# Kernel optimization log

Measured on AMD Instinct MI355X. Metric: run time of the kernel, lower is better.

## Reference

```python
import jax, jax.numpy as jnp
import numpy as np


def _soft_proto(x, P):
    d2 = (x * x).sum(-1, keepdims=True) - 2.0 * (x @ P.T) + (P * P).sum(-1)
    w = jax.nn.softmax(-d2, axis=-1)  # scores = -dist_sq, softmax over K
    return w @ P  # soft-matched prototypes


def setup_inputs() -> dict:
    key = jax.random.key(0)
    ks = jax.random.split(key, 12)
    B = 1024
    def u(k, shape, s=0.1):
        return jax.random.uniform(k, shape, minval=-s, maxval=s, dtype=jnp.float32)
    return {
        "fcn": jax.random.normal(ks[0], (B, 90, 90), jnp.float32),
        "scn": jax.random.normal(ks[1], (B, 90, 90), jnp.float32),
        # node embedding Linear(90->48), weights stored [in,out]
        "W_node": u(ks[2], (90, 48)), "b_node": jnp.zeros((48,), jnp.float32),
        "P_node": u(ks[3], (64, 48)),   # node prototypes, init uniform(-0.1,0.1)
        "W_graph": u(ks[4], (48, 32)), "b_graph": jnp.zeros((32,), jnp.float32),
        "P_graph": u(ks[5], (32, 32)),
        "Wg1": u(ks[6], (32, 32)), "bg1": jnp.zeros((32,), jnp.float32),
        "Wg2": u(ks[7], (32, 16)), "bg2": jnp.zeros((16,), jnp.float32),
        "P_cls": u(ks[8], (16, 16)),
        # classifier: final_dim = 2*90*48 + 2*32 + 2*16 = 8736
        "Wc1": u(ks[9], (8736, 256)), "bc1": jnp.zeros((256,), jnp.float32),
        "Wc2": u(ks[10], (256, 3)), "bc2": jnp.zeros((3,), jnp.float32),
    }


def reference(fcn, scn, W_node, b_node, P_node, W_graph, b_graph, P_graph,
              Wg1, bg1, Wg2, bg2, P_cls, Wc1, bc1, Wc2, bc2):
    def branch(x):
        nodes = x @ W_node + b_node                  # [B,90,48]
        nm = _soft_proto(nodes, P_node)              # [B,90,48]
        eg = nm.mean(axis=1) @ W_graph + b_graph     # [B,32]
        gp = _soft_proto(eg, P_graph)                # [B,32]
        ec = jax.nn.relu(gp @ Wg1 + bg1) @ Wg2 + bg2 # [B,16]
        cp = _soft_proto(ec, P_cls)                  # [B,16]
        return nm, gp, cp

    nmf, gpf, cpf = branch(fcn)
    nms, gps, cps = branch(scn)
    B = fcn.shape[0]
    R = jnp.concatenate(
        [nmf.reshape(B, -1), nms.reshape(B, -1), gpf, gps, cpf, cps], axis=-1)  # [B,8736]
    # dropout(0.5) is identity in eval mode
    logits = jax.nn.relu(R @ Wc1 + bc1) @ Wc2 + bc2  # [B,3]
    return logits
```

## Files before the change

### kernel.cpp

```cpp
#include <hip/hip_runtime.h>
#include <hip/hip_bf16.h>

using f16   = _Float16;
using f16x4 = __attribute__((ext_vector_type(4))) _Float16;
using f16x8 = __attribute__((ext_vector_type(8))) _Float16;
using f32x4 = __attribute__((ext_vector_type(4))) float;

__global__ __launch_bounds__(256) void prep_kernel(
    const float* __restrict__ Wn, const float* __restrict__ Pn,
    f16* __restrict__ wf, float* __restrict__ q)
{
  int i = blockIdx.x * 256 + threadIdx.x;
  if (i < 4992) {
    int n = i / 104, k = i - n * 104;
    wf[i] = (k < 90) ? (f16)Wn[k * 48 + n] : (f16)0.f;
  } else if (i < 8576) {
    int j = i - 4992; int p = j / 56, c = j - p * 56;
    wf[i] = (c < 48) ? (f16)Pn[p * 48 + c] : (f16)0.f;
  } else if (i < 12032) {
    int j = i - 8576; int r = j / 72, p = j - r * 72;
    wf[i] = (p < 64) ? (f16)Pn[p * 48 + r] : (f16)0.f;
  } else if (i < 12096) {
    int p = i - 12032;
    float s = 0.f;
    for (int j = 0; j < 48; ++j) { float v = Pn[p * 48 + j]; s = fmaf(v, v, s); }
    q[p] = s;
  }
}

__global__ __launch_bounds__(256) void wc1t_kernel(
    const float* __restrict__ Wc1, f16* __restrict__ Wc1T)
{
  __shared__ f16 sT[32 * 36];
  const int tid = threadIdx.x;
  const int kt = blockIdx.x, ct = blockIdx.y;
  const int c = tid & 31, r4 = (tid >> 5) * 4;
  #pragma unroll
  for (int i = 0; i < 4; ++i) {
    int r = r4 + i;
    sT[c * 36 + r] = (f16)Wc1[(size_t)(kt * 32 + r) * 256 + ct * 32 + c];
  }
  __syncthreads();
  #pragma unroll
  for (int i = 0; i < 4; ++i) {
    int r = r4 + i;
    Wc1T[(size_t)(ct * 32 + r) * 8736 + kt * 32 + c] = sT[r * 36 + c];
  }
}

__global__ __launch_bounds__(384) void node_kernel(
    const float* __restrict__ fcn, const float* __restrict__ scn,
    const float* __restrict__ bn, const f16* __restrict__ wf,
    const float* __restrict__ qg,
    f16* __restrict__ R, float* __restrict__ nmmean)
{
  __shared__ __align__(16) f16 sWt[12032];
  __shared__ __align__(16) f16 sS[6][1152];
  __shared__ float sCol[6][3][16];

  f16* sWnT = sWt;
  f16* sP   = sWt + 4992;
  f16* sPnT = sWt + 8576;

  const int tid = threadIdx.x;
  const int lane = tid & 63, wv = tid >> 6;
  const int l15 = lane & 15, lg = lane >> 4;
  const int b = blockIdx.x, br = blockIdx.y;
  const float* x = (br ? scn : fcn) + (size_t)b * 8100;
  f16* scr = sS[wv];

  const int row = wv * 16 + l15;
  const float* xrow = x + row * 90;
  float2 xl[3][4];
  #pragma unroll
  for (int kt = 0; kt < 3; ++kt) {
    #pragma unroll
    for (int e = 0; e < 4; ++e) xl[kt][e] = make_float2(0.f, 0.f);
    const int k0 = kt * 32 + lg * 8;
    if (row < 90) {
      const float* src = xrow + k0;
      if (k0 < 88) {
        xl[kt][0] = *(const float2*)(src + 0);
        xl[kt][1] = *(const float2*)(src + 2);
        xl[kt][2] = *(const float2*)(src + 4);
        xl[kt][3] = *(const float2*)(src + 6);
      } else {
        xl[kt][0] = *(const float2*)src;
      }
    }
  }

  for (int i = tid; i < 1504; i += 384)
    ((f16x8*)sWt)[i] = ((const f16x8*)wf)[i];
  __syncthreads();

  f16x8 a[3];
  #pragma unroll
  for (int kt = 0; kt < 3; ++kt) {
    f16x8 h;
    h[0] = (f16)xl[kt][0].x; h[1] = (f16)xl[kt][0].y;
    h[2] = (f16)xl[kt][1].x; h[3] = (f16)xl[kt][1].y;
    h[4] = (f16)xl[kt][2].x; h[5] = (f16)xl[kt][2].y;
    h[6] = (f16)xl[kt][3].x; h[7] = (f16)xl[kt][3].y;
    a[kt] = h;
  }

  #pragma unroll
  for (int nt = 0; nt < 3; ++nt) {
    f32x4 acc = {0.f, 0.f, 0.f, 0.f};
    #pragma unroll
    for (int kt = 0; kt < 3; ++kt) {
      f16x8 bb = *(const f16x8*)&sWnT[(nt * 16 + l15) * 104 + kt * 32 + lg * 8];
      acc = __builtin_amdgcn_mfma_f32_16x16x32_f16(a[kt], bb, acc, 0, 0, 0);
    }
    const float bias = bn[nt * 16 + l15];
    #pragma unroll
    for (int r = 0; r < 4; ++r)
      scr[(lg * 4 + r) * 56 + nt * 16 + l15] = (f16)(acc[r] + bias);
  }
  asm volatile("s_waitcnt lgkmcnt(0)" ::: "memory");
  __builtin_amdgcn_sched_barrier(0);

  const f16x8 a0 = *(const f16x8*)&scr[l15 * 56 + lg * 8];
  const f16x4 a1 = *(const f16x4*)&scr[l15 * 56 + 32 + lg * 4];
  f32x4 acc2[4];
  #pragma unroll
  for (int nt = 0; nt < 4; ++nt) acc2[nt] = (f32x4){0.f, 0.f, 0.f, 0.f};
  #pragma unroll
  for (int nt = 0; nt < 4; ++nt) {
    f16x8 b0 = *(const f16x8*)&sP[(nt * 16 + l15) * 56 + lg * 8];
    acc2[nt] = __builtin_amdgcn_mfma_f32_16x16x32_f16(a0, b0, acc2[nt], 0, 0, 0);
    f16x4 b1 = *(const f16x4*)&sP[(nt * 16 + l15) * 56 + 32 + lg * 4];
    acc2[nt] = __builtin_amdgcn_mfma_f32_16x16x16f16(a1, b1, acc2[nt], 0, 0, 0);
  }
  float qv[4];
  #pragma unroll
  for (int nt = 0; nt < 4; ++nt) qv[nt] = qg[nt * 16 + l15];
  #pragma unroll
  for (int r = 0; r < 4; ++r) {
    float s0 = 2.f * acc2[0][r] - qv[0];
    float s1 = 2.f * acc2[1][r] - qv[1];
    float s2 = 2.f * acc2[2][r] - qv[2];
    float s3 = 2.f * acc2[3][r] - qv[3];
    float m = fmaxf(fmaxf(s0, s1), fmaxf(s2, s3));
    m = fmaxf(m, __shfl_xor(m, 1, 64));
    m = fmaxf(m, __shfl_xor(m, 2, 64));
    m = fmaxf(m, __shfl_xor(m, 4, 64));
    m = fmaxf(m, __shfl_xor(m, 8, 64));
    float e0 = __expf(s0 - m), e1 = __expf(s1 - m);
    float e2 = __expf(s2 - m), e3 = __expf(s3 - m);
    float sum = (e0 + e1) + (e2 + e3);
    sum += __shfl_xor(sum, 1, 64);
    sum += __shfl_xor(sum, 2, 64);
    sum += __shfl_xor(sum, 4, 64);
    sum += __shfl_xor(sum, 8, 64);
    const float inv = 1.f / sum;
    const int lr = lg * 4 + r;
    scr[lr * 72 + 0 * 16 + l15] = (f16)(e0 * inv);
    scr[lr * 72 + 1 * 16 + l15] = (f16)(e1 * inv);
    scr[lr * 72 + 2 * 16 + l15] = (f16)(e2 * inv);
    scr[lr * 72 + 3 * 16 + l15] = (f16)(e3 * inv);
  }
  asm volatile("s_waitcnt lgkmcnt(0)" ::: "memory");
  __builtin_amdgcn_sched_barrier(0);

  f16* Rrow = R + (size_t)b * 8736 + (size_t)br * 4320;
  const f16x8 wa0 = *(const f16x8*)&scr[l15 * 72 + lg * 8];
  const f16x8 wa1 = *(const f16x8*)&scr[l15 * 72 + 32 + lg * 8];
  float cs[3] = {0.f, 0.f, 0.f};
  #pragma unroll
  for (int nt = 0; nt < 3; ++nt) {
    f32x4 acc = {0.f, 0.f, 0.f, 0.f};
    f16x8 b0 = *(const f16x8*)&sPnT[(nt * 16 + l15) * 72 + lg * 8];
    acc = __builtin_amdgcn_mfma_f32_16x16x32_f16(wa0, b0, acc, 0, 0, 0);
    f16x8 b1 = *(const f16x8*)&sPnT[(nt * 16 + l15) * 72 + 32 + lg * 8];
    acc = __builtin_amdgcn_mfma_f32_16x16x32_f16(wa1, b1, acc, 0, 0, 0);
    #pragma unroll
    for (int r = 0; r < 4; ++r) {
      const int grow = wv * 16 + lg * 4 + r;
      if (grow < 90) {
        Rrow[grow * 48 + nt * 16 + l15] = (f16)acc[r];
        cs[nt] += acc[r];
      }
    }
  }
  #pragma unroll
  for (int nt = 0; nt < 3; ++nt) {
    cs[nt] += __shfl_xor(cs[nt], 16, 64);
    cs[nt] += __shfl_xor(cs[nt], 32, 64);
  }
  if (lane < 16) {
    sCol[wv][0][lane] = cs[0];
    sCol[wv][1][lane] = cs[1];
    sCol[wv][2][lane] = cs[2];
  }
  __syncthreads();
  if (tid < 48) {
    const int nt = tid >> 4, c = tid & 15;
    float s = 0.f;
    #pragma unroll
    for (int w = 0; w < 6; ++w) s += sCol[w][nt][c];
    nmmean[((size_t)br * 1024 + b) * 48 + tid] = s * (1.f / 90.f);
  }
}

__global__ __launch_bounds__(256) void graph_kernel(
    const float* __restrict__ nmmean,
    const float* __restrict__ Wg, const float* __restrict__ bg,
    const float* __restrict__ Pg,
    const float* __restrict__ Wg1, const float* __restrict__ bg1,
    const float* __restrict__ Wg2, const float* __restrict__ bg2,
    const float* __restrict__ Pc,
    f16* __restrict__ R)
{
  __shared__ float sE[4][64];
  __shared__ float sT[4][64];
  const int tid = threadIdx.x;
  const int wid = tid >> 6, lane = tid & 63;
  const int idx = blockIdx.x * 4 + wid;
  const int br = idx >> 10, b = idx & 1023;
  const float* mrow = nmmean + (size_t)idx * 48;
  f16* Rrow = R + (size_t)b * 8736;

  if (lane < 32) {
    float e = bg[lane];
    #pragma unroll
    for (int k = 0; k < 48; ++k) e = fmaf(mrow[k], Wg[k * 32 + lane], e);
    sE[wid][lane] = e;
  }
  __syncthreads();
  if (lane < 32) {
    float s = 0.f;
    #pragma unroll
    for (int j = 0; j < 32; ++j) { float pv = Pg[lane * 32 + j]; s += pv * (2.f * sE[wid][j] - pv); }
    float m = s;
    for (int d = 16; d >= 1; d >>= 1) m = fmaxf(m, __shfl_xor(m, d, 64));
    float ex = __expf(s - m);
    float sum = ex;
    for (int d = 16; d >= 1; d >>= 1) sum += __shfl_xor(sum, d, 64);
    sT[wid][lane] = ex / sum;
  }
  __syncthreads();
  if (lane < 32) {
    float g = 0.f;
    #pragma unroll
    for (int p = 0; p < 32; ++p) g = fmaf(sT[wid][p], Pg[p * 32 + lane], g);
    Rrow[8640 + br * 32 + lane] = (f16)g;
    sE[wid][lane] = g;
  }
  __syncthreads();
  if (lane < 32) {
    float h = bg1[lane];
    #pragma unroll
    for (int k = 0; k < 32; ++k) h = fmaf(sE[wid][k], Wg1[k * 32 + lane], h);
    sT[wid][lane] = fmaxf(h, 0.f);
  }
  __syncthreads();
  if (lane < 16) {
    float c = bg2[lane];
    #pragma unroll
    for (int k = 0; k < 32; ++k) c = fmaf(sT[wid][k], Wg2[k * 16 + lane], c);
    sE[wid][lane] = c;
  }
  __syncthreads();
  if (lane < 16) {
    float s = 0.f;
    #pragma unroll
    for (int j = 0; j < 16; ++j) { float pv = Pc[lane * 16 + j]; s += pv * (2.f * sE[wid][j] - pv); }
    float m = s;
    for (int d = 8; d >= 1; d >>= 1) m = fmaxf(m, __shfl_xor(m, d, 64));
    float ex = __expf(s - m);
    float sum = ex;
    for (int d = 8; d >= 1; d >>= 1) sum += __shfl_xor(sum, d, 64);
    sT[wid][lane] = ex / sum;
  }
  __syncthreads();
  if (lane < 16) {
    float c = 0.f;
    #pragma unroll
    for (int p = 0; p < 16; ++p) c = fmaf(sT[wid][p], Pc[p * 16 + lane], c);
    Rrow[8704 + br * 16 + lane] = (f16)c;
  }
}

__global__ __launch_bounds__(256) void gemm1_kernel(
    const f16* __restrict__ R, const f16* __restrict__ Wc1T,
    float* __restrict__ part, int KS)
{
  __shared__ __align__(16) f16 sA[128 * 40];
  __shared__ __align__(16) f16 sB[64 * 40];
  const int tid = threadIdx.x;
  const int lane = tid & 63, wv = tid >> 6;
  const int l15 = lane & 15, lg = lane >> 4;
  const int wm = wv >> 1, wn = wv & 1;
  const int bm = blockIdx.x * 128, bnc = blockIdx.y * 64, z = blockIdx.z;
  const int base = 273 / KS, rem = 273 - base * KS;
  const int t0 = z * base + (z < rem ? z : rem);
  const int nt_ = base + (z < rem ? 1 : 0);
  const int kbeg = t0 * 32, kend = (t0 + nt_) * 32;

  const int ar = tid >> 1, ah = (tid & 1) * 16;
  const int bc = tid >> 2, bh = (tid & 3) * 8;

  f32x4 acc[4][2];
  #pragma unroll
  for (int mt = 0; mt < 4; ++mt)
    #pragma unroll
    for (int nt = 0; nt < 2; ++nt) acc[mt][nt] = (f32x4){0.f, 0.f, 0.f, 0.f};

  f16x8 v0 = *(const f16x8*)&R[(size_t)(bm + ar) * 8736 + kbeg + ah];
  f16x8 v1 = *(const f16x8*)&R[(size_t)(bm + ar) * 8736 + kbeg + ah + 8];
  f16x8 w0 = *(const f16x8*)&Wc1T[(size_t)(bnc + bc) * 8736 + kbeg + bh];

  for (int kk = kbeg; kk < kend; kk += 32) {
    *(f16x8*)&sA[ar * 40 + ah] = v0;
    *(f16x8*)&sA[ar * 40 + ah + 8] = v1;
    *(f16x8*)&sB[bc * 40 + bh] = w0;
    __syncthreads();
    if (kk + 32 < kend) {
      v0 = *(const f16x8*)&R[(size_t)(bm + ar) * 8736 + kk + 32 + ah];
      v1 = *(const f16x8*)&R[(size_t)(bm + ar) * 8736 + kk + 32 + ah + 8];
      w0 = *(const f16x8*)&Wc1T[(size_t)(bnc + bc) * 8736 + kk + 32 + bh];
    }
    #pragma unroll
    for (int mt = 0; mt < 4; ++mt) {
      f16x8 a = *(const f16x8*)&sA[(wm * 64 + mt * 16 + l15) * 40 + lg * 8];
      #pragma unroll
      for (int nt = 0; nt < 2; ++nt) {
        f16x8 bb = *(const f16x8*)&sB[(wn * 32 + nt * 16 + l15) * 40 + lg * 8];
        acc[mt][nt] = __builtin_amdgcn_mfma_f32_16x16x32_f16(a, bb, acc[mt][nt], 0, 0, 0);
      }
    }
    __syncthreads();
  }
  float* pz = part + (size_t)z * 262144;
  #pragma unroll
  for (int mt = 0; mt < 4; ++mt)
    #pragma unroll
    for (int nt = 0; nt < 2; ++nt)
      #pragma unroll
      for (int r = 0; r < 4; ++r)
        pz[(size_t)(bm + wm * 64 + mt * 16 + lg * 4 + r) * 256 +
           bnc + wn * 32 + nt * 16 + l15] = acc[mt][nt][r];
}

__global__ __launch_bounds__(256) void head_kernel(
    const float* __restrict__ part, const float* __restrict__ bc1,
    const float* __restrict__ Wc2, const float* __restrict__ bc2,
    float* __restrict__ out, int KS)
{
  __shared__ float red[3][4];
  const int b = blockIdx.x, t = threadIdx.x;
  float s0 = 0.f, s1 = 0.f, s2 = 0.f, s3 = 0.f;
  int z = 0;
  for (; z + 4 <= KS; z += 4) {
    s0 += part[(size_t)(z + 0) * 262144 + (size_t)b * 256 + t];
    s1 += part[(size_t)(z + 1) * 262144 + (size_t)b * 256 + t];
    s2 += part[(size_t)(z + 2) * 262144 + (size_t)b * 256 + t];
    s3 += part[(size_t)(z + 3) * 262144 + (size_t)b * 256 + t];
  }
  for (; z < KS; ++z) s0 += part[(size_t)z * 262144 + (size_t)b * 256 + t];
  float acc = bc1[t] + ((s0 + s1) + (s2 + s3));
  float h = fmaxf(acc, 0.f);
  float p0 = h * Wc2[t * 3 + 0];
  float p1 = h * Wc2[t * 3 + 1];
  float p2 = h * Wc2[t * 3 + 2];
  for (int d = 32; d >= 1; d >>= 1) {
    p0 += __shfl_xor(p0, d, 64);
    p1 += __shfl_xor(p1, d, 64);
    p2 += __shfl_xor(p2, d, 64);
  }
  const int wid = t >> 6, lane = t & 63;
  if (lane == 0) { red[0][wid] = p0; red[1][wid] = p1; red[2][wid] = p2; }
  __syncthreads();
  if (t < 3) {
    out[(size_t)b * 3 + t] = red[t][0] + red[t][1] + red[t][2] + red[t][3] + bc2[t];
  }
}

extern "C" void kernel_launch(void* const* d_in, const int* in_sizes, int n_in,
                              void* d_out, int out_size, void* d_ws, size_t ws_size,
                              hipStream_t stream) {
  const float* fcn     = (const float*)d_in[0];
  const float* scn     = (const float*)d_in[1];
  const float* W_node  = (const float*)d_in[2];
  const float* b_node  = (const float*)d_in[3];
  const float* P_node  = (const float*)d_in[4];
  const float* W_graph = (const float*)d_in[5];
  const float* b_graph = (const float*)d_in[6];
  const float* P_graph = (const float*)d_in[7];
  const float* Wg1     = (const float*)d_in[8];
  const float* bg1     = (const float*)d_in[9];
  const float* Wg2     = (const float*)d_in[10];
  const float* bg2     = (const float*)d_in[11];
  const float* P_cls   = (const float*)d_in[12];
  const float* Wc1     = (const float*)d_in[13];
  const float* bc1     = (const float*)d_in[14];
  const float* Wc2     = (const float*)d_in[15];
  const float* bc2     = (const float*)d_in[16];
  float* out = (float*)d_out;

  char* ws = (char*)d_ws;
  f16*   R16    = (f16*)ws;
  f16*   Wc1T   = (f16*)(ws + 17891328);
  f16*   wf     = (f16*)(ws + 22364160);
  float* qbuf   = (float*)(ws + 22388224);
  float* nmmean = (float*)(ws + 22388480);
  float* part   = (float*)(ws + 22781696);

  size_t avail = ws_size > 22781696u ? ws_size - 22781696u : 0;
  int KS = (int)(avail / 1048576u);
  if (KS > 16) KS = 16;
  if (KS < 1) KS = 1;

  prep_kernel<<<48, 256, 0, stream>>>(W_node, P_node, wf, qbuf);
  wc1t_kernel<<<dim3(273, 8), 256, 0, stream>>>(Wc1, Wc1T);
  node_kernel<<<dim3(1024, 2), 384, 0, stream>>>(fcn, scn, b_node, wf, qbuf,
                                                 R16, nmmean);
  graph_kernel<<<512, 256, 0, stream>>>(nmmean, W_graph, b_graph, P_graph,
                                        Wg1, bg1, Wg2, bg2, P_cls, R16);
  gemm1_kernel<<<dim3(8, 4, KS), 256, 0, stream>>>(R16, Wc1T, part, KS);
  head_kernel<<<1024, 256, 0, stream>>>(part, bc1, Wc2, bc2, out, KS);
}
```

Baseline: 68.61 us.

## Merge independent kernels into horizontal fat launches and move graph/cls terms to head

Merges the Wc1 transpose into the node kernel as extra blocks, and the graph/proto kernel into the split-K GEMM kernel as extra blocks. This removes launches and lets independent work share the GPU. To break the dependency of the GEMM on the graph outputs, the GEMM now covers only the first 270 K-tiles (the node features). The remaining 96 classifier columns are computed in fp32 inside the head kernel from a new gcp buffer. The transpose blocks now run with 384-thread blocks where only 256 threads work, and the head kernel does extra strided Wc1 reads per row.

Measured after the change: 68.61 us. No clear change (-0.0%).

```diff
diff --git a/kernel.cpp b/kernel.cpp
--- a/kernel.cpp
+++ b/kernel.cpp
@@ -28,44 +28,49 @@
   }
 }
 
-__global__ __launch_bounds__(256) void wc1t_kernel(
-    const float* __restrict__ Wc1, f16* __restrict__ Wc1T)
-{
-  __shared__ f16 sT[32 * 36];
-  const int tid = threadIdx.x;
-  const int kt = blockIdx.x, ct = blockIdx.y;
-  const int c = tid & 31, r4 = (tid >> 5) * 4;
-  #pragma unroll
-  for (int i = 0; i < 4; ++i) {
-    int r = r4 + i;
-    sT[c * 36 + r] = (f16)Wc1[(size_t)(kt * 32 + r) * 256 + ct * 32 + c];
-  }
-  __syncthreads();
-  #pragma unroll
-  for (int i = 0; i < 4; ++i) {
-    int r = r4 + i;
-    Wc1T[(size_t)(ct * 32 + r) * 8736 + kt * 32 + c] = sT[r * 36 + c];
-  }
-}
-
-__global__ __launch_bounds__(384) void node_kernel(
+__global__ __launch_bounds__(384) void fat1_kernel(
     const float* __restrict__ fcn, const float* __restrict__ scn,
     const float* __restrict__ bn, const f16* __restrict__ wf,
     const float* __restrict__ qg,
+    const float* __restrict__ Wc1, f16* __restrict__ Wc1T,
     f16* __restrict__ R, float* __restrict__ nmmean)
 {
   __shared__ __align__(16) f16 sWt[12032];
   __shared__ __align__(16) f16 sS[6][1152];
   __shared__ float sCol[6][3][16];
 
+  const int blk = blockIdx.x;
+  const int tid = threadIdx.x;
+
+  if (blk < 2184) {
+    f16* sT = sWt;
+    const int kt = blk % 273, ct = blk / 273;
+    const int c = tid & 31, r4 = (tid >> 5) * 4;
+    if (tid < 256) {
+      #pragma unroll
+      for (int i = 0; i < 4; ++i) {
+        int r = r4 + i;
+        sT[c * 36 + r] = (f16)Wc1[(size_t)(kt * 32 + r) * 256 + ct * 32 + c];
+      }
+    }
+    __syncthreads();
+    if (tid < 256) {
+      #pragma unroll
+      for (int i = 0; i < 4; ++i) {
+        int r = r4 + i;
+        Wc1T[(size_t)(ct * 32 + r) * 8736 + kt * 32 + c] = sT[r * 36 + c];
+      }
+    }
+    return;
+  }
+
+  const int unit = blk - 2184;
+  const int b = unit & 1023, br = unit >> 10;
   f16* sWnT = sWt;
   f16* sP   = sWt + 4992;
   f16* sPnT = sWt + 8576;
-
-  const int tid = threadIdx.x;
   const int lane = tid & 63, wv = tid >> 6;
   const int l15 = lane & 15, lg = lane >> 4;
-  const int b = blockIdx.x, br = blockIdx.y;
   const float* x = (br ? scn : fcn) + (size_t)b * 8100;
   f16* scr = sS[wv];
 
@@ -204,97 +209,102 @@
   }
 }
 
-__global__ __launch_bounds__(256) void graph_kernel(
+__global__ __launch_bounds__(256) void fat2_kernel(
     const float* __restrict__ nmmean,
     const float* __restrict__ Wg, const float* __restrict__ bg,
     const float* __restrict__ Pg,
     const float* __restrict__ Wg1, const float* __restrict__ bg1,
     const float* __restrict__ Wg2, const float* __restrict__ bg2,
     const float* __restrict__ Pc,
-    f16* __restrict__ R)
-{
-  __shared__ float sE[4][64];
-  __shared__ float sT[4][64];
-  const int tid = threadIdx.x;
-  const int wid = tid >> 6, lane = tid & 63;
-  const int idx = blockIdx.x * 4 + wid;
-  const int br = idx >> 10, b = idx & 1023;
-  const float* mrow = nmmean + (size_t)idx * 48;
-  f16* Rrow = R + (size_t)b * 8736;
-
-  if (lane < 32) {
-    float e = bg[lane];
-    #pragma unroll
-    for (int k = 0; k < 48; ++k) e = fmaf(mrow[k], Wg[k * 32 + lane], e);
-    sE[wid][lane] = e;
-  }
-  __syncthreads();
-  if (lane < 32) {
-    float s = 0.f;
-    #pragma unroll
-    for (int j = 0; j < 32; ++j) { float pv = Pg[lane * 32 + j]; s += pv * (2.f * sE[wid][j] - pv); }
-    float m = s;
-    for (int d = 16; d >= 1; d >>= 1) m = fmaxf(m, __shfl_xor(m, d, 64));
-    float ex = __expf(s - m);
-    float sum = ex;
-    for (int d = 16; d >= 1; d >>= 1) sum += __shfl_xor(sum, d, 64);
-    sT[wid][lane] = ex / sum;
-  }
-  __syncthreads();
-  if (lane < 32) {
-    float g = 0.f;
-    #pragma unroll
-    for (int p = 0; p < 32; ++p) g = fmaf(sT[wid][p], Pg[p * 32 + lane], g);
-    Rrow[8640 + br * 32 + lane] = (f16)g;
-    sE[wid][lane] = g;
-  }
-  __syncthreads();
-  if (lane < 32) {
-    float h = bg1[lane];
-    #pragma unroll
-    for (int k = 0; k < 32; ++k) h = fmaf(sE[wid][k], Wg1[k * 32 + lane], h);
-    sT[wid][lane] = fmaxf(h, 0.f);
-  }
-  __syncthreads();
-  if (lane < 16) {
-    float c = bg2[lane];
-    #pragma unroll
-    for (int k = 0; k < 32; ++k) c = fmaf(sT[wid][k], Wg2[k * 16 + lane], c);
-    sE[wid][lane] = c;
-  }
-  __syncthreads();
-  if (lane < 16) {
-    float s = 0.f;
-    #pragma unroll
-    for (int j = 0; j < 16; ++j) { float pv = Pc[lane * 16 + j]; s += pv * (2.f * sE[wid][j] - pv); }
-    float m = s;
-    for (int d = 8; d >= 1; d >>= 1) m = fmaxf(m, __shfl_xor(m, d, 64));
-    float ex = __expf(s - m);
-    float sum = ex;
-    for (int d = 8; d >= 1; d >>= 1) sum += __shfl_xor(sum, d, 64);
-    sT[wid][lane] = ex / sum;
-  }
-  __syncthreads();
-  if (lane < 16) {
-    float c = 0.f;
-    #pragma unroll
-    for (int p = 0; p < 16; ++p) c = fmaf(sT[wid][p], Pc[p * 16 + lane], c);
-    Rrow[8704 + br * 16 + lane] = (f16)c;
-  }
-}
-
-__global__ __launch_bounds__(256) void gemm1_kernel(
+    float* __restrict__ gcp,
     const f16* __restrict__ R, const f16* __restrict__ Wc1T,
     float* __restrict__ part, int KS)
 {
   __shared__ __align__(16) f16 sA[128 * 40];
   __shared__ __align__(16) f16 sB[64 * 40];
+
+  const int blk = blockIdx.x;
   const int tid = threadIdx.x;
+
+  if (blk < 512) {
+    float (*sE)[64] = (float(*)[64])sA;
+    float (*sT)[64] = (float(*)[64])(sA + 512);
+    const int wid = tid >> 6, lane = tid & 63;
+    const int idx = blk * 4 + wid;
+    const int br = idx >> 10, b = idx & 1023;
+    const float* mrow = nmmean + (size_t)idx * 48;
+    float* grow = gcp + (size_t)idx * 48;
+
+    if (lane < 32) {
+      float e = bg[lane];
+      #pragma unroll
+      for (int k = 0; k < 48; ++k) e = fmaf(mrow[k], Wg[k * 32 + lane], e);
+      sE[wid][lane] = e;
+    }
+    __syncthreads();
+    if (lane < 32) {
+      float s = 0.f;
+      #pragma unroll
+      for (int j = 0; j < 32; ++j) { float pv = Pg[lane * 32 + j]; s += pv * (2.f * sE[wid][j] - pv); }
+      float m = s;
+      for (int d = 16; d >= 1; d >>= 1) m = fmaxf(m, __shfl_xor(m, d, 64));
+      float ex = __expf(s - m);
+      float sum = ex;
+      for (int d = 16; d >= 1; d >>= 1) sum += __shfl_xor(sum, d, 64);
+      sT[wid][lane] = ex / sum;
+    }
+    __syncthreads();
+    if (lane < 32) {
+      float g = 0.f;
+      #pragma unroll
+      for (int p = 0; p < 32; ++p) g = fmaf(sT[wid][p], Pg[p * 32 + lane], g);
+      grow[lane] = g;
+      sE[wid][lane] = g;
+    }
+    __syncthreads();
+    if (lane < 32) {
+      float h = bg1[lane];
+      #pragma unroll
+      for (int k = 0; k < 32; ++k) h = fmaf(sE[wid][k], Wg1[k * 32 + lane], h);
+      sT[wid][lane] = fmaxf(h, 0.f);
+    }
+    __syncthreads();
+    if (lane < 16) {
+      float c = bg2[lane];
+      #pragma unroll
+      for (int k = 0; k < 32; ++k) c = fmaf(sT[wid][k], Wg2[k * 16 + lane], c);
+      sE[wid][lane] = c;
+    }
+    __syncthreads();
+    if (lane < 16) {
+      float s = 0.f;
+      #pragma unroll
+      for (int j = 0; j < 16; ++j) { float pv = Pc[lane * 16 + j]; s += pv * (2.f * sE[wid][j] - pv); }
+      float m = s;
+      for (int d = 8; d >= 1; d >>= 1) m = fmaxf(m, __shfl_xor(m, d, 64));
+      float ex = __expf(s - m);
+      float sum = ex;
+      for (int d = 8; d >= 1; d >>= 1) sum += __shfl_xor(sum, d, 64);
+      sT[wid][lane] = ex / sum;
+    }
+    __syncthreads();
+    if (lane < 16) {
+      float c = 0.f;
+      #pragma unroll
+      for (int p = 0; p < 16; ++p) c = fmaf(sT[wid][p], Pc[p * 16 + lane], c);
+      grow[32 + lane] = c;
+    }
+    return;
+  }
+
+  const int flat = blk - 512;
+  const int z = flat >> 5;
+  const int r5 = flat & 31;
+  const int bm = (r5 >> 2) * 128, bnc = (r5 & 3) * 64;
   const int lane = tid & 63, wv = tid >> 6;
   const int l15 = lane & 15, lg = lane >> 4;
   const int wm = wv >> 1, wn = wv & 1;
-  const int bm = blockIdx.x * 128, bnc = blockIdx.y * 64, z = blockIdx.z;
-  const int base = 273 / KS, rem = 273 - base * KS;
+  const int base = 270 / KS, rem = 270 - base * KS;
   const int t0 = z * base + (z < rem ? z : rem);
   const int nt_ = base + (z < rem ? 1 : 0);
   const int kbeg = t0 * 32, kend = (t0 + nt_) * 32;
@@ -345,7 +355,8 @@
 }
 
 __global__ __launch_bounds__(256) void head_kernel(
-    const float* __restrict__ part, const float* __restrict__ bc1,
+    const float* __restrict__ part, const float* __restrict__ gcp,
+    const float* __restrict__ Wc1, const float* __restrict__ bc1,
     const float* __restrict__ Wc2, const float* __restrict__ bc2,
     float* __restrict__ out, int KS)
 {
@@ -361,6 +372,22 @@
   }
   for (; z < KS; ++z) s0 += part[(size_t)z * 262144 + (size_t)b * 256 + t];
   float acc = bc1[t] + ((s0 + s1) + (s2 + s3));
+
+  const float* g0 = gcp + (size_t)b * 48;
+  const float* g1 = gcp + (size_t)(1024 + b) * 48;
+  #pragma unroll 8
+  for (int k = 0; k < 32; ++k)
+    acc = fmaf(g0[k], Wc1[(size_t)(8640 + k) * 256 + t], acc);
+  #pragma unroll 8
+  for (int k = 0; k < 32; ++k)
+    acc = fmaf(g1[k], Wc1[(size_t)(8672 + k) * 256 + t], acc);
+  #pragma unroll 8
+  for (int k = 0; k < 16; ++k)
+    acc = fmaf(g0[32 + k], Wc1[(size_t)(8704 + k) * 256 + t], acc);
+  #pragma unroll 8
+  for (int k = 0; k < 16; ++k)
+    acc = fmaf(g1[32 + k], Wc1[(size_t)(8720 + k) * 256 + t], acc);
+
   float h = fmaxf(acc, 0.f);
   float p0 = h * Wc2[t * 3 + 0];
   float p1 = h * Wc2[t * 3 + 1];
@@ -406,19 +433,19 @@
   f16*   wf     = (f16*)(ws + 22364160);
   float* qbuf   = (float*)(ws + 22388224);
   float* nmmean = (float*)(ws + 22388480);
-  float* part   = (float*)(ws + 22781696);
-
-  size_t avail = ws_size > 22781696u ? ws_size - 22781696u : 0;
+  float* gcp    = (float*)(ws + 22781696);
+  float* part   = (float*)(ws + 23174912);
+
+  size_t avail = ws_size > 23174912u ? ws_size - 23174912u : 0;
   int KS = (int)(avail / 1048576u);
   if (KS > 16) KS = 16;
   if (KS < 1) KS = 1;
 
   prep_kernel<<<48, 256, 0, stream>>>(W_node, P_node, wf, qbuf);
-  wc1t_kernel<<<dim3(273, 8), 256, 0, stream>>>(Wc1, Wc1T);
-  node_kernel<<<dim3(1024, 2), 384, 0, stream>>>(fcn, scn, b_node, wf, qbuf,
-                                                 R16, nmmean);
-  graph_kernel<<<512, 256, 0, stream>>>(nmmean, W_graph, b_graph, P_graph,
-                                        Wg1, bg1, Wg2, bg2, P_cls, R16);
-  gemm1_kernel<<<dim3(8, 4, KS), 256, 0, stream>>>(R16, Wc1T, part, KS);
-  head_kernel<<<1024, 256, 0, stream>>>(part, bc1, Wc2, bc2, out, KS);
+  fat1_kernel<<<2184 + 2048, 384, 0, stream>>>(fcn, scn, b_node, wf, qbuf,
+                                               Wc1, Wc1T, R16, nmmean);
+  fat2_kernel<<<512 + 32 * KS, 256, 0, stream>>>(nmmean, W_graph, b_graph, P_graph,
+                                                 Wg1, bg1, Wg2, bg2, P_cls, gcp,
+                                                 R16, Wc1T, part, KS);
+  head_kernel<<<1024, 256, 0, stream>>>(part, gcp, Wc1, bc1, Wc2, bc2, out, KS);
 }
```
